# Kernel optimization log

Hardware: AMD Instinct MI355X
Metric: run time of the kernel (lower is better)

## Reference

```python
import jax, jax.numpy as jnp
import numpy as np

DIM = 1024
NUM_HEADS = 16
HEAD_DIM = 64  # DIM // NUM_HEADS
BATCH = 2
SEQ = 2048


def setup_inputs() -> dict:
    key = jax.random.key(0)
    ks = jax.random.split(key, 6)
    x = jax.random.normal(ks[0], (BATCH, SEQ, DIM), dtype=jnp.float32)
    # Linear weights stored as [in, out] so y = x @ W (same math as torch Linear).
    Wq = jax.random.normal(ks[1], (DIM, DIM), dtype=jnp.float32) * (DIM ** -0.5)
    # MQA: single shared KV head of size HEAD_DIM.
    Wk = jax.random.normal(ks[2], (DIM, HEAD_DIM), dtype=jnp.float32) * (DIM ** -0.5)
    Wv = jax.random.normal(ks[3], (DIM, HEAD_DIM), dtype=jnp.float32) * (DIM ** -0.5)
    Wo = jax.random.normal(ks[4], (DIM, DIM), dtype=jnp.float32) * (DIM ** -0.5)
    bo = jax.random.normal(ks[5], (DIM,), dtype=jnp.float32) * 0.01
    return {"x": x, "Wq": Wq, "Wk": Wk, "Wv": Wv, "Wo": Wo, "bo": bo}


def reference(x, Wq, Wk, Wv, Wo, bo):
    b, s, _ = x.shape
    scale = HEAD_DIM ** -0.5
    # Per-head queries [b, h, s, d]
    q = (x @ Wq).reshape(b, s, NUM_HEADS, HEAD_DIM).transpose(0, 2, 1, 3) * scale
    # Shared single KV head [b, s, d]
    k = x @ Wk
    v = x @ Wv
    # Materialized scores [b, h, s_q, s_k]
    scores = jnp.einsum('bhqd,bkd->bhqk', q, k)
    causal = jnp.tril(jnp.ones((s, s), dtype=bool))  # True where allowed
    scores = jnp.where(causal, scores, -jnp.inf)
    # Manual stable softmax (max, exp, sum, div) as in the original
    max_scores = jnp.max(scores, axis=-1, keepdims=True)
    exp_scores = jnp.exp(scores - max_scores)
    attn = exp_scores / jnp.sum(exp_scores, axis=-1, keepdims=True)
    out = jnp.einsum('bhqk,bkd->bhqd', attn, v)  # [b, h, s, d]
    out = out.transpose(0, 2, 1, 3).reshape(b, s, DIM)
    return out @ Wo + bo
```

## Files before the change

### kernel.cpp

```cpp
#include <hip/hip_runtime.h>

typedef unsigned short u16;
typedef __attribute__((ext_vector_type(8))) short short8;
typedef __attribute__((ext_vector_type(4))) float f32x4;

static __device__ __forceinline__ u16 f32_to_bf16(float f) {
  unsigned u = __float_as_uint(f);
  u += 0x7fffu + ((u >> 16) & 1u);
  return (u16)(u >> 16);
}

static __device__ __forceinline__ void async16(u16* lds, const u16* g) {
  __builtin_amdgcn_global_load_lds(
      (const __attribute__((address_space(1))) void*)g,
      (__attribute__((address_space(3))) void*)lds, 16, 0, 0);
}


__global__ void __launch_bounds__(256) convert_kernel(
    const float* __restrict__ x, u16* __restrict__ Xb) {
  int t = blockIdx.x * 256 + threadIdx.x;
  int base = t * 8;
  float4 a = *(const float4*)&x[base];
  float4 b = *(const float4*)&x[base + 4];
  short8 v;
  v[0] = (short)f32_to_bf16(a.x); v[1] = (short)f32_to_bf16(a.y);
  v[2] = (short)f32_to_bf16(a.z); v[3] = (short)f32_to_bf16(a.w);
  v[4] = (short)f32_to_bf16(b.x); v[5] = (short)f32_to_bf16(b.y);
  v[6] = (short)f32_to_bf16(b.z); v[7] = (short)f32_to_bf16(b.w);
  *(short8*)&Xb[base] = v;
}

__global__ void __launch_bounds__(256) transpose_kernel(
    const float* __restrict__ Wq, const float* __restrict__ Wk,
    const float* __restrict__ Wv, const float* __restrict__ Wo,
    u16* __restrict__ WqT, u16* __restrict__ WkvT, u16* __restrict__ WoT) {
  __shared__ u16 T[64][72];
  int id = blockIdx.x;
  const float* src; u16* dst; int tk, tn, src_ld, row_off;
  if (id < 256)      { src = Wq; dst = WqT;  tk = id & 15;  tn = id >> 4; src_ld = 1024; row_off = 0; }
  else if (id < 512) { int i = id - 256; src = Wo; dst = WoT; tk = i & 15; tn = i >> 4; src_ld = 1024; row_off = 0; }
  else if (id < 528) { src = Wk; dst = WkvT; tk = id - 512; tn = 0; src_ld = 64; row_off = 0; }
  else               { src = Wv; dst = WkvT; tk = id - 528; tn = 0; src_ld = 64; row_off = 64; }
  int k0 = tk * 64, n0 = tn * 64;
  int tid = threadIdx.x;
#pragma unroll
  for (int it = 0; it < 2; ++it) {
    int c = tid + it * 256;
    int r = c >> 3, cc = (c & 7) * 8;
    const float* p = &src[(k0 + r) * src_ld + n0 + cc];
    float4 a = *(const float4*)&p[0];
    float4 b = *(const float4*)&p[4];
    short8 v;
    v[0] = (short)f32_to_bf16(a.x); v[1] = (short)f32_to_bf16(a.y);
    v[2] = (short)f32_to_bf16(a.z); v[3] = (short)f32_to_bf16(a.w);
    v[4] = (short)f32_to_bf16(b.x); v[5] = (short)f32_to_bf16(b.y);
    v[6] = (short)f32_to_bf16(b.z); v[7] = (short)f32_to_bf16(b.w);
    *(short8*)&T[r][cc] = v;
  }
  __syncthreads();
#pragma unroll
  for (int it = 0; it < 2; ++it) {
    int c = tid + it * 256;
    int r = c >> 3, cc = (c & 7) * 8;
    short8 v;
#pragma unroll
    for (int j = 0; j < 8; ++j) v[j] = (short)T[cc + j][r];
    *(short8*)&dst[(row_off + n0 + r) * 1024 + k0 + cc] = v;
  }
}

__device__ __forceinline__ void gemm_core_128(
    const u16* __restrict__ A, const u16* __restrict__ BT, int m0, int K,
    f32x4 (&acc)[4][4], u16* As, u16* Bs,
    int lane, int w, int wr, int wc, int g, int lo) {
  int lrow = lane >> 3;
  int swz8 = ((lane & 7) ^ lrow) * 8;
  int lo7 = lo & 7;
  for (int k0 = 0; k0 < K; k0 += 64) {
#pragma unroll
    for (int it = 0; it < 4; ++it) {
      int W = w * 4 + it;
      int row = W * 8 + lrow;
      async16(As + W * 512, &A[(size_t)(m0 + row) * K + k0 + swz8]);
      async16(Bs + W * 512, &BT[(size_t)row * K + k0 + swz8]);
    }
    __syncthreads();
#pragma unroll
    for (int ks = 0; ks < 2; ++ks) {
      short8 af[4], bf[4];
#pragma unroll
      for (int i = 0; i < 4; ++i) {
        int pc = ((ks * 4 + g) ^ lo7) * 8;
        af[i] = *(const short8*)&As[(wr * 64 + i * 16 + lo) * 64 + pc];
        bf[i] = *(const short8*)&Bs[(wc * 64 + i * 16 + lo) * 64 + pc];
      }
#pragma unroll
      for (int mi = 0; mi < 4; ++mi)
#pragma unroll
        for (int ni = 0; ni < 4; ++ni)
          acc[mi][ni] = __builtin_amdgcn_mfma_f32_16x16x32_bf16(
              af[mi], bf[ni], acc[mi][ni], 0, 0, 0);
    }
    __syncthreads();
  }
}

__global__ void __launch_bounds__(256) qkv_gemm(
    const u16* __restrict__ Xb, const u16* __restrict__ WqT,
    const u16* __restrict__ WkvT, u16* __restrict__ Qb, u16* __restrict__ KVb,
    u16* __restrict__ VTb) {
  __shared__ u16 As[128 * 64];
  __shared__ u16 Bs[128 * 64];
  int tid = threadIdx.x, lane = tid & 63, w = tid >> 6;
  int wr = w >> 1, wc = w & 1, g = lane >> 4, lo = lane & 15;
  int m0 = blockIdx.x * 128, nb = blockIdx.y;
  const u16* BT = (nb < 8) ? (WqT + (size_t)nb * 128 * 1024) : WkvT;
  f32x4 acc[4][4];
  f32x4 zz = {0.f, 0.f, 0.f, 0.f};
#pragma unroll
  for (int i = 0; i < 4; ++i)
#pragma unroll
    for (int j = 0; j < 4; ++j) acc[i][j] = zz;
  gemm_core_128(Xb, BT, m0, 1024, acc, As, Bs, lane, w, wr, wc, g, lo);
#pragma unroll
  for (int mi = 0; mi < 4; ++mi)
#pragma unroll
    for (int ni = 0; ni < 4; ++ni)
#pragma unroll
      for (int r = 0; r < 4; ++r) {
        int row = m0 + wr * 64 + mi * 16 + g * 4 + r;
        int col = wc * 64 + ni * 16 + lo;
        u16 v = f32_to_bf16(acc[mi][ni][r]);
        if (nb < 8) {
          Qb[row * 1024 + nb * 128 + col] = v;
        } else if (wc == 0) {
          KVb[row * 64 + col] = v;
        } else {
          int d = col - 64;
          VTb[(((row >> 11) * 64) + d) * 2048 + (row & 2047)] = v;
        }
      }
}

__global__ void __launch_bounds__(256, 4) attn_kernel(
    const u16* __restrict__ Qb, const u16* __restrict__ KVb,
    const u16* __restrict__ VTb, u16* __restrict__ AOb) {
  __shared__ u16 Ks[64 * 64];
  __shared__ u16 Vt[64 * 64];
  __shared__ u16 Ps[4][16][72];
  int tid = threadIdx.x, lane = tid & 63, w = tid >> 6;
  int g = lane >> 4, lo = lane & 15;
  int h = blockIdx.x;
  int by = blockIdx.y;
  int qt = (by < 16) ? by : (47 - by);
  int b = blockIdx.z;
  int q0 = qt * 64;
  int qbase = q0 + w * 16;
  int lrow = lane >> 3;
  int swz8 = ((lane & 7) ^ lrow) * 8;
  int lo7 = lo & 7;

  short8 qf[2];
  {
    const u16* qp = &Qb[(size_t)(b * 2048 + qbase + lo) * 1024 + h * 64];
    qf[0] = *(const short8*)&qp[g * 8];
    qf[1] = *(const short8*)&qp[32 + g * 8];
  }

  short8 ones;
#pragma unroll
  for (int j = 0; j < 8; ++j) ones[j] = (short)0x3F80;

  f32x4 oacc[4], l_acc;
  f32x4 zz = {0.f, 0.f, 0.f, 0.f};
#pragma unroll
  for (int i = 0; i < 4; ++i) oacc[i] = zz;
  l_acc = zz;

  const float kExp = 0.18033688011112042f;
  const float kOff = 11.541560327111707f;

  int ntiles = qt + 1;
  for (int t = 0; t < ntiles; ++t) {
    int k0 = t * 64;
#pragma unroll
    for (int it = 0; it < 2; ++it) {
      int W = w * 2 + it;
      async16(Ks + W * 512, &KVb[(size_t)(b * 2048 + k0 + W * 8 + lrow) * 64 + swz8]);
      async16(Vt + W * 512, &VTb[((size_t)b * 64 + W * 8 + lrow) * 2048 + k0 + swz8]);
    }
    __syncthreads();

    f32x4 sacc[4];
#pragma unroll
    for (int ns = 0; ns < 4; ++ns) sacc[ns] = zz;
#pragma unroll
    for (int ks = 0; ks < 2; ++ks) {
      short8 kf[4];
      int pc = ((ks * 4 + g) ^ lo7) * 8;
#pragma unroll
      for (int ns = 0; ns < 4; ++ns)
        kf[ns] = *(const short8*)&Ks[(ns * 16 + lo) * 64 + pc];
#pragma unroll
      for (int ns = 0; ns < 4; ++ns)
        sacc[ns] = __builtin_amdgcn_mfma_f32_16x16x32_bf16(
            qf[ks], kf[ns], sacc[ns], 0, 0, 0);
    }

    bool need_mask = (k0 + 63) > qbase;
#pragma unroll
    for (int ns = 0; ns < 4; ++ns)
#pragma unroll
      for (int r = 0; r < 4; ++r) {
        float p = __builtin_amdgcn_exp2f(fmaf(sacc[ns][r], kExp, -kOff));
        if (need_mask) {
          int qg = qbase + g * 4 + r;
          int kg = k0 + ns * 16 + lo;
          if (kg > qg) p = 0.f;
        }
        Ps[w][g * 4 + r][ns * 16 + lo] = f32_to_bf16(p);
      }
    __syncthreads();

#pragma unroll
    for (int k2 = 0; k2 < 2; ++k2) {
      short8 pf = *(const short8*)&Ps[w][lo][k2 * 32 + g * 8];
      short8 vf[4];
      int pc = ((k2 * 4 + g) ^ lo7) * 8;
#pragma unroll
      for (int ds = 0; ds < 4; ++ds)
        vf[ds] = *(const short8*)&Vt[(ds * 16 + lo) * 64 + pc];
#pragma unroll
      for (int ds = 0; ds < 4; ++ds)
        oacc[ds] = __builtin_amdgcn_mfma_f32_16x16x32_bf16(
            pf, vf[ds], oacc[ds], 0, 0, 0);
      l_acc = __builtin_amdgcn_mfma_f32_16x16x32_bf16(pf, ones, l_acc, 0, 0, 0);
    }
    __syncthreads();
  }

#pragma unroll
  for (int r = 0; r < 4; ++r) {
    float inv_l = 1.0f / l_acc[r];
    int row = b * 2048 + qbase + g * 4 + r;
#pragma unroll
    for (int ds = 0; ds < 4; ++ds)
      AOb[row * 1024 + h * 64 + ds * 16 + lo] = f32_to_bf16(oacc[ds][r] * inv_l);
  }
}

__global__ void __launch_bounds__(256) out_gemm(
    const u16* __restrict__ A, const u16* __restrict__ WoT,
    const float* __restrict__ bias, float* __restrict__ C) {
  __shared__ u16 As[128 * 64];
  __shared__ u16 Bs[128 * 64];
  int tid = threadIdx.x, lane = tid & 63, w = tid >> 6;
  int wr = w >> 1, wc = w & 1, g = lane >> 4, lo = lane & 15;
  int m0 = blockIdx.x * 128, nb = blockIdx.y;
  const u16* BT = WoT + (size_t)nb * 128 * 1024;
  f32x4 acc[4][4];
  f32x4 zz = {0.f, 0.f, 0.f, 0.f};
#pragma unroll
  for (int i = 0; i < 4; ++i)
#pragma unroll
    for (int j = 0; j < 4; ++j) acc[i][j] = zz;
  gemm_core_128(A, BT, m0, 1024, acc, As, Bs, lane, w, wr, wc, g, lo);
#pragma unroll
  for (int mi = 0; mi < 4; ++mi)
#pragma unroll
    for (int ni = 0; ni < 4; ++ni)
#pragma unroll
      for (int r = 0; r < 4; ++r) {
        int row = m0 + wr * 64 + mi * 16 + g * 4 + r;
        int col = nb * 128 + wc * 64 + ni * 16 + lo;
        C[row * 1024 + col] = acc[mi][ni][r] + bias[col];
      }
}

extern "C" void kernel_launch(void* const* d_in, const int* in_sizes, int n_in,
                              void* d_out, int out_size, void* d_ws, size_t ws_size,
                              hipStream_t stream) {
  const float* x  = (const float*)d_in[0];
  const float* Wq = (const float*)d_in[1];
  const float* Wk = (const float*)d_in[2];
  const float* Wv = (const float*)d_in[3];
  const float* Wo = (const float*)d_in[4];
  const float* bo = (const float*)d_in[5];
  float* out = (float*)d_out;

  u16* ws   = (u16*)d_ws;
  u16* AOb  = ws;
  u16* KVb  = AOb + 4194304;
  u16* VTb  = KVb + 262144;
  u16* Xb   = VTb + 262144;
  u16* WqT  = Xb + 4194304;
  u16* WoT  = WqT + 1048576;
  u16* WkvT = WoT + 1048576;
  u16* Qb   = (u16*)d_out;

  convert_kernel<<<2048, 256, 0, stream>>>(x, Xb);
  transpose_kernel<<<544, 256, 0, stream>>>(Wq, Wk, Wv, Wo, WqT, WkvT, WoT);
  qkv_gemm<<<dim3(32, 9), 256, 0, stream>>>(Xb, WqT, WkvT, Qb, KVb, VTb);
  attn_kernel<<<dim3(16, 32, 2), 256, 0, stream>>>(Qb, KVb, VTb, AOb);
  out_gemm<<<dim3(32, 8), 256, 0, stream>>>(AOb, WoT, bo, out);
}
```

Baseline: 175.9 us.

## Double-buffer LDS tiles in GEMMs and attention, merge prep kernels

Result: no change. 174.1 us (-1.0%).

```diff
diff --git a/kernel.cpp b/kernel.cpp
--- a/kernel.cpp
+++ b/kernel.cpp
@@ -17,33 +17,34 @@
 }
 
 
-__global__ void __launch_bounds__(256) convert_kernel(
-    const float* __restrict__ x, u16* __restrict__ Xb) {
-  int t = blockIdx.x * 256 + threadIdx.x;
-  int base = t * 8;
-  float4 a = *(const float4*)&x[base];
-  float4 b = *(const float4*)&x[base + 4];
-  short8 v;
-  v[0] = (short)f32_to_bf16(a.x); v[1] = (short)f32_to_bf16(a.y);
-  v[2] = (short)f32_to_bf16(a.z); v[3] = (short)f32_to_bf16(a.w);
-  v[4] = (short)f32_to_bf16(b.x); v[5] = (short)f32_to_bf16(b.y);
-  v[6] = (short)f32_to_bf16(b.z); v[7] = (short)f32_to_bf16(b.w);
-  *(short8*)&Xb[base] = v;
-}
-
-__global__ void __launch_bounds__(256) transpose_kernel(
+__global__ void __launch_bounds__(256) prep_kernel(
+    const float* __restrict__ x,
     const float* __restrict__ Wq, const float* __restrict__ Wk,
     const float* __restrict__ Wv, const float* __restrict__ Wo,
-    u16* __restrict__ WqT, u16* __restrict__ WkvT, u16* __restrict__ WoT) {
+    u16* __restrict__ Xb, u16* __restrict__ WqT, u16* __restrict__ WkvT,
+    u16* __restrict__ WoT) {
   __shared__ u16 T[64][72];
   int id = blockIdx.x;
+  int tid = threadIdx.x;
+  if (id < 2048) {
+    int base = (id * 256 + tid) * 8;
+    float4 a = *(const float4*)&x[base];
+    float4 b = *(const float4*)&x[base + 4];
+    short8 v;
+    v[0] = (short)f32_to_bf16(a.x); v[1] = (short)f32_to_bf16(a.y);
+    v[2] = (short)f32_to_bf16(a.z); v[3] = (short)f32_to_bf16(a.w);
+    v[4] = (short)f32_to_bf16(b.x); v[5] = (short)f32_to_bf16(b.y);
+    v[6] = (short)f32_to_bf16(b.z); v[7] = (short)f32_to_bf16(b.w);
+    *(short8*)&Xb[base] = v;
+    return;
+  }
+  int id2 = id - 2048;
   const float* src; u16* dst; int tk, tn, src_ld, row_off;
-  if (id < 256)      { src = Wq; dst = WqT;  tk = id & 15;  tn = id >> 4; src_ld = 1024; row_off = 0; }
-  else if (id < 512) { int i = id - 256; src = Wo; dst = WoT; tk = i & 15; tn = i >> 4; src_ld = 1024; row_off = 0; }
-  else if (id < 528) { src = Wk; dst = WkvT; tk = id - 512; tn = 0; src_ld = 64; row_off = 0; }
-  else               { src = Wv; dst = WkvT; tk = id - 528; tn = 0; src_ld = 64; row_off = 64; }
+  if (id2 < 256)      { src = Wq; dst = WqT;  tk = id2 & 15; tn = id2 >> 4; src_ld = 1024; row_off = 0; }
+  else if (id2 < 512) { int i = id2 - 256; src = Wo; dst = WoT; tk = i & 15; tn = i >> 4; src_ld = 1024; row_off = 0; }
+  else if (id2 < 528) { src = Wk; dst = WkvT; tk = id2 - 512; tn = 0; src_ld = 64; row_off = 0; }
+  else                { src = Wv; dst = WkvT; tk = id2 - 528; tn = 0; src_ld = 64; row_off = 64; }
   int k0 = tk * 64, n0 = tn * 64;
-  int tid = threadIdx.x;
 #pragma unroll
   for (int it = 0; it < 2; ++it) {
     int c = tid + it * 256;
@@ -70,30 +71,42 @@
   }
 }
 
-__device__ __forceinline__ void gemm_core_128(
+__device__ __forceinline__ void stage_128(
+    const u16* __restrict__ A, const u16* __restrict__ BT, int m0, int K,
+    int k0, u16* As, u16* Bs, int w, int lrow, int swz8) {
+#pragma unroll
+  for (int it = 0; it < 4; ++it) {
+    int W = w * 4 + it;
+    async16(As + W * 512, &A[(size_t)(m0 + W * 8 + lrow) * K + k0 + swz8]);
+    async16(Bs + W * 512, &BT[(size_t)(W * 8 + lrow) * K + k0 + swz8]);
+  }
+}
+
+__device__ __forceinline__ void gemm_core_128_db(
     const u16* __restrict__ A, const u16* __restrict__ BT, int m0, int K,
     f32x4 (&acc)[4][4], u16* As, u16* Bs,
     int lane, int w, int wr, int wc, int g, int lo) {
   int lrow = lane >> 3;
   int swz8 = ((lane & 7) ^ lrow) * 8;
   int lo7 = lo & 7;
-  for (int k0 = 0; k0 < K; k0 += 64) {
-#pragma unroll
-    for (int it = 0; it < 4; ++it) {
-      int W = w * 4 + it;
-      int row = W * 8 + lrow;
-      async16(As + W * 512, &A[(size_t)(m0 + row) * K + k0 + swz8]);
-      async16(Bs + W * 512, &BT[(size_t)row * K + k0 + swz8]);
-    }
+  const int NK = K >> 6;
+  stage_128(A, BT, m0, K, 0, As, Bs, w, lrow, swz8);
+  for (int kt = 0; kt < NK; ++kt) {
+    int cur = kt & 1;
     __syncthreads();
+    if (kt + 1 < NK)
+      stage_128(A, BT, m0, K, (kt + 1) * 64,
+                As + (cur ^ 1) * 8192, Bs + (cur ^ 1) * 8192, w, lrow, swz8);
+    const u16* Asc = As + cur * 8192;
+    const u16* Bsc = Bs + cur * 8192;
 #pragma unroll
     for (int ks = 0; ks < 2; ++ks) {
+      int pc = ((ks * 4 + g) ^ lo7) * 8;
       short8 af[4], bf[4];
 #pragma unroll
       for (int i = 0; i < 4; ++i) {
-        int pc = ((ks * 4 + g) ^ lo7) * 8;
-        af[i] = *(const short8*)&As[(wr * 64 + i * 16 + lo) * 64 + pc];
-        bf[i] = *(const short8*)&Bs[(wc * 64 + i * 16 + lo) * 64 + pc];
+        af[i] = *(const short8*)&Asc[(wr * 64 + i * 16 + lo) * 64 + pc];
+        bf[i] = *(const short8*)&Bsc[(wc * 64 + i * 16 + lo) * 64 + pc];
       }
 #pragma unroll
       for (int mi = 0; mi < 4; ++mi)
@@ -102,7 +115,6 @@
           acc[mi][ni] = __builtin_amdgcn_mfma_f32_16x16x32_bf16(
               af[mi], bf[ni], acc[mi][ni], 0, 0, 0);
     }
-    __syncthreads();
   }
 }
 
@@ -110,8 +122,8 @@
     const u16* __restrict__ Xb, const u16* __restrict__ WqT,
     const u16* __restrict__ WkvT, u16* __restrict__ Qb, u16* __restrict__ KVb,
     u16* __restrict__ VTb) {
-  __shared__ u16 As[128 * 64];
-  __shared__ u16 Bs[128 * 64];
+  __shared__ u16 As[2 * 128 * 64];
+  __shared__ u16 Bs[2 * 128 * 64];
   int tid = threadIdx.x, lane = tid & 63, w = tid >> 6;
   int wr = w >> 1, wc = w & 1, g = lane >> 4, lo = lane & 15;
   int m0 = blockIdx.x * 128, nb = blockIdx.y;
@@ -122,7 +134,7 @@
   for (int i = 0; i < 4; ++i)
 #pragma unroll
     for (int j = 0; j < 4; ++j) acc[i][j] = zz;
-  gemm_core_128(Xb, BT, m0, 1024, acc, As, Bs, lane, w, wr, wc, g, lo);
+  gemm_core_128_db(Xb, BT, m0, 1024, acc, As, Bs, lane, w, wr, wc, g, lo);
 #pragma unroll
   for (int mi = 0; mi < 4; ++mi)
 #pragma unroll
@@ -143,14 +155,14 @@
       }
 }
 
-__global__ void __launch_bounds__(256, 4) attn_kernel(
+__global__ void __launch_bounds__(256) attn_kernel(
     const u16* __restrict__ Qb, const u16* __restrict__ KVb,
     const u16* __restrict__ VTb, u16* __restrict__ AOb) {
-  __shared__ u16 Ks[64 * 64];
-  __shared__ u16 Vt[64 * 64];
+  __shared__ u16 Ks[2][64 * 64];
+  __shared__ u16 Vt[2][64 * 64];
   __shared__ u16 Ps[4][16][72];
   int tid = threadIdx.x, lane = tid & 63, w = tid >> 6;
-  int g = lane >> 4, lo = lane & 15;
+  int gq = lane >> 4, lo = lane & 15;
   int h = blockIdx.x;
   int by = blockIdx.y;
   int qt = (by < 16) ? by : (47 - by);
@@ -164,16 +176,16 @@
   short8 qf[2];
   {
     const u16* qp = &Qb[(size_t)(b * 2048 + qbase + lo) * 1024 + h * 64];
-    qf[0] = *(const short8*)&qp[g * 8];
-    qf[1] = *(const short8*)&qp[32 + g * 8];
+    qf[0] = *(const short8*)&qp[gq * 8];
+    qf[1] = *(const short8*)&qp[32 + gq * 8];
   }
 
   short8 ones;
 #pragma unroll
   for (int j = 0; j < 8; ++j) ones[j] = (short)0x3F80;
 
+  f32x4 zz = {0.f, 0.f, 0.f, 0.f};
   f32x4 oacc[4], l_acc;
-  f32x4 zz = {0.f, 0.f, 0.f, 0.f};
 #pragma unroll
   for (int i = 0; i < 4; ++i) oacc[i] = zz;
   l_acc = zz;
@@ -181,69 +193,76 @@
   const float kExp = 0.18033688011112042f;
   const float kOff = 11.541560327111707f;
 
-  int ntiles = qt + 1;
-  for (int t = 0; t < ntiles; ++t) {
-    int k0 = t * 64;
+  auto stage_kv = [&](int t, int bu) {
 #pragma unroll
     for (int it = 0; it < 2; ++it) {
       int W = w * 2 + it;
-      async16(Ks + W * 512, &KVb[(size_t)(b * 2048 + k0 + W * 8 + lrow) * 64 + swz8]);
-      async16(Vt + W * 512, &VTb[((size_t)b * 64 + W * 8 + lrow) * 2048 + k0 + swz8]);
+      async16(&Ks[bu][W * 512],
+              &KVb[(size_t)(b * 2048 + t * 64 + W * 8 + lrow) * 64 + swz8]);
+      async16(&Vt[bu][W * 512],
+              &VTb[((size_t)b * 64 + W * 8 + lrow) * 2048 + t * 64 + swz8]);
     }
+  };
+
+  int nst = qt + 1;
+  stage_kv(0, 0);
+  for (int t = 0; t < nst; ++t) {
+    int cur = t & 1;
     __syncthreads();
+    if (t + 1 < nst) stage_kv(t + 1, cur ^ 1);
+    int k0 = t * 64;
 
     f32x4 sacc[4];
 #pragma unroll
     for (int ns = 0; ns < 4; ++ns) sacc[ns] = zz;
 #pragma unroll
     for (int ks = 0; ks < 2; ++ks) {
+      int pc = ((ks * 4 + gq) ^ lo7) * 8;
       short8 kf[4];
-      int pc = ((ks * 4 + g) ^ lo7) * 8;
 #pragma unroll
       for (int ns = 0; ns < 4; ++ns)
-        kf[ns] = *(const short8*)&Ks[(ns * 16 + lo) * 64 + pc];
+        kf[ns] = *(const short8*)&Ks[cur][(ns * 16 + lo) * 64 + pc];
 #pragma unroll
       for (int ns = 0; ns < 4; ++ns)
         sacc[ns] = __builtin_amdgcn_mfma_f32_16x16x32_bf16(
             qf[ks], kf[ns], sacc[ns], 0, 0, 0);
     }
 
-    bool need_mask = (k0 + 63) > qbase;
+    bool diag = (t == qt);
 #pragma unroll
     for (int ns = 0; ns < 4; ++ns)
 #pragma unroll
       for (int r = 0; r < 4; ++r) {
         float p = __builtin_amdgcn_exp2f(fmaf(sacc[ns][r], kExp, -kOff));
-        if (need_mask) {
-          int qg = qbase + g * 4 + r;
+        if (diag) {
+          int qg = qbase + gq * 4 + r;
           int kg = k0 + ns * 16 + lo;
           if (kg > qg) p = 0.f;
         }
-        Ps[w][g * 4 + r][ns * 16 + lo] = f32_to_bf16(p);
+        Ps[w][gq * 4 + r][ns * 16 + lo] = (u16)(__float_as_uint(p) >> 16);
       }
-    __syncthreads();
+    __threadfence_block();
 
 #pragma unroll
     for (int k2 = 0; k2 < 2; ++k2) {
-      short8 pf = *(const short8*)&Ps[w][lo][k2 * 32 + g * 8];
+      short8 pf = *(const short8*)&Ps[w][lo][k2 * 32 + gq * 8];
+      int pc = ((k2 * 4 + gq) ^ lo7) * 8;
       short8 vf[4];
-      int pc = ((k2 * 4 + g) ^ lo7) * 8;
 #pragma unroll
       for (int ds = 0; ds < 4; ++ds)
-        vf[ds] = *(const short8*)&Vt[(ds * 16 + lo) * 64 + pc];
+        vf[ds] = *(const short8*)&Vt[cur][(ds * 16 + lo) * 64 + pc];
 #pragma unroll
       for (int ds = 0; ds < 4; ++ds)
         oacc[ds] = __builtin_amdgcn_mfma_f32_16x16x32_bf16(
             pf, vf[ds], oacc[ds], 0, 0, 0);
       l_acc = __builtin_amdgcn_mfma_f32_16x16x32_bf16(pf, ones, l_acc, 0, 0, 0);
     }
-    __syncthreads();
   }
 
 #pragma unroll
   for (int r = 0; r < 4; ++r) {
     float inv_l = 1.0f / l_acc[r];
-    int row = b * 2048 + qbase + g * 4 + r;
+    int row = b * 2048 + qbase + gq * 4 + r;
 #pragma unroll
     for (int ds = 0; ds < 4; ++ds)
       AOb[row * 1024 + h * 64 + ds * 16 + lo] = f32_to_bf16(oacc[ds][r] * inv_l);
@@ -253,8 +272,8 @@
 __global__ void __launch_bounds__(256) out_gemm(
     const u16* __restrict__ A, const u16* __restrict__ WoT,
     const float* __restrict__ bias, float* __restrict__ C) {
-  __shared__ u16 As[128 * 64];
-  __shared__ u16 Bs[128 * 64];
+  __shared__ u16 As[2 * 128 * 64];
+  __shared__ u16 Bs[2 * 128 * 64];
   int tid = threadIdx.x, lane = tid & 63, w = tid >> 6;
   int wr = w >> 1, wc = w & 1, g = lane >> 4, lo = lane & 15;
   int m0 = blockIdx.x * 128, nb = blockIdx.y;
@@ -265,7 +284,7 @@
   for (int i = 0; i < 4; ++i)
 #pragma unroll
     for (int j = 0; j < 4; ++j) acc[i][j] = zz;
-  gemm_core_128(A, BT, m0, 1024, acc, As, Bs, lane, w, wr, wc, g, lo);
+  gemm_core_128_db(A, BT, m0, 1024, acc, As, Bs, lane, w, wr, wc, g, lo);
 #pragma unroll
   for (int mi = 0; mi < 4; ++mi)
 #pragma unroll
@@ -299,8 +318,7 @@
   u16* WkvT = WoT + 1048576;
   u16* Qb   = (u16*)d_out;
 
-  convert_kernel<<<2048, 256, 0, stream>>>(x, Xb);
-  transpose_kernel<<<544, 256, 0, stream>>>(Wq, Wk, Wv, Wo, WqT, WkvT, WoT);
+  prep_kernel<<<2592, 256, 0, stream>>>(x, Wq, Wk, Wv, Wo, Xb, WqT, WkvT, WoT);
   qkv_gemm<<<dim3(32, 9), 256, 0, stream>>>(Xb, WqT, WkvT, Qb, KVb, VTb);
   attn_kernel<<<dim3(16, 32, 2), 256, 0, stream>>>(Qb, KVb, VTb, AOb);
   out_gemm<<<dim3(32, 8), 256, 0, stream>>>(AOb, WoT, bo, out);
```
